# Performance work log

Measured on AMD Instinct MI355X. Metric: run time of the kernel, lower is better.

The kernel has to match this reference:

```python
import jax, jax.numpy as jnp
import numpy as np

IN_F = 512
OUT_F = 512
ALPHA = 0.2  # LeakyReLU negative slope
# dropout p=0.1 is a no-op at inference (training=False), so omitted


def setup_inputs() -> dict:
    key = jax.random.key(0)
    k1, k2, k3 = jax.random.split(key, 3)
    B, N = 16, 1024
    x = jax.random.normal(k1, (B, N, IN_F), dtype=jnp.float32)
    # xavier_uniform with gain=1.414
    limW = 1.414 * np.sqrt(6.0 / (IN_F + OUT_F))
    W = jax.random.uniform(k2, (IN_F, OUT_F), minval=-limW, maxval=limW, dtype=jnp.float32)
    lima = 1.414 * np.sqrt(6.0 / (2 * OUT_F + 1))
    a = jax.random.uniform(k3, (2 * OUT_F, 1), minval=-lima, maxval=lima, dtype=jnp.float32)
    beta = jnp.ones((1,), dtype=jnp.float32)
    return {"x": x, "W": W, "a": a, "beta": beta}


def reference(x, W, a, beta):
    # h: [B, N, F]
    h = jnp.matmul(x, W)
    # Split attention vector: e_ij = leakyrelu(h_i . a1 + h_j . a2)
    a1 = a[:OUT_F, 0]   # [F]
    a2 = a[OUT_F:, 0]   # [F]
    s1 = jnp.einsum('bnf,f->bn', h, a1)  # [B, N]
    s2 = jnp.einsum('bnf,f->bn', h, a2)  # [B, N]
    e = s1[:, :, None] + s2[:, None, :]  # [B, N, N]
    e = jnp.where(e > 0, e, ALPHA * e)   # LeakyReLU
    attention = jax.nn.softmax(e, axis=2)
    h_prime = jnp.einsum('bnm,bmf->bnf', attention, h)
    out = jax.nn.elu(h_prime + beta * h)
    return out
```

## Files before the change

### kernel.cpp

```cpp
#include <hip/hip_runtime.h>

using u16 = unsigned short;
using u32 = unsigned int;

#define ALPHA 0.2f
#define LOG2E 1.4426950408889634f

typedef __bf16 bf16x8 __attribute__((ext_vector_type(8)));
typedef float f32x4 __attribute__((ext_vector_type(4)));
typedef float f32x16 __attribute__((ext_vector_type(16)));

__device__ __forceinline__ u16 f2bf(float f) {
  u32 u = __builtin_bit_cast(u32, f);
  u += 0x7FFFu + ((u >> 16) & 1u);
  return (u16)(u >> 16);
}
__device__ __forceinline__ float bf2f(u16 h) {
  u32 u = ((u32)h) << 16;
  return __builtin_bit_cast(float, u);
}
__device__ __forceinline__ void gload_lds16(const void* g, void* l) {
  __builtin_amdgcn_global_load_lds((__attribute__((address_space(1))) void*)g,
                                   (__attribute__((address_space(3))) void*)l,
                                   16, 0, 0);
}

__global__ __launch_bounds__(256) void k_cast_wT(const float* __restrict__ W, u16* __restrict__ wbt) {
  int idx = blockIdx.x * 256 + threadIdx.x;
  int k = idx >> 9, n = idx & 511;
  wbt[n * 512 + k] = f2bf(W[idx]);
}


__global__ __launch_bounds__(256, 2) void k_gemm1(const float* __restrict__ x, const u16* __restrict__ wbt,
                                                  const float* __restrict__ a,
                                                  u16* __restrict__ hbf, u16* __restrict__ hbt2,
                                                  float* __restrict__ s1p, float* __restrict__ s2p) {
  __shared__ __attribute__((aligned(16))) char lds[73728];
  __shared__ __attribute__((aligned(16))) float a_l[256];

  const int t = threadIdx.x;
  const int lane = t & 63;
  const int w = t >> 6;
  const int l31 = lane & 31, lhi = lane >> 5;
  const int rb = w >> 1, cg = w & 1;
  const int g = blockIdx.x;
  const int cb = (g >> 3) & 3;
  const int tile_m = (g & 7) | ((g >> 5) << 3);
  const int row0 = tile_m * 128;
  const int col0 = cb * 128;

  a_l[t] = (t < 128) ? a[col0 + t] : a[512 + col0 + (t - 128)];

  f32x16 acc[2][2];
#pragma unroll
  for (int i = 0; i < 2; ++i)
#pragma unroll
    for (int j = 0; j < 2; ++j)
#pragma unroll
      for (int r = 0; r < 16; ++r) acc[i][j][r] = 0.f;

#define STAGE_G1(kt, Ab, Bb)                                                              \
  {                                                                                       \
    const int k0_ = (kt) * 32;                                                            \
    _Pragma("unroll")                                                                     \
    for (int i = 0; i < 4; ++i) {                                                         \
      int G = i * 256 + t;                                                                \
      int row = G >> 3, ks = G & 7;                                                       \
      gload_lds16(x + (size_t)(row0 + row) * 512 + k0_ + ((ks ^ (row & 7)) * 4),          \
                  (Ab) + (size_t)(i * 256 + w * 64) * 16);                                \
    }                                                                                     \
    _Pragma("unroll")                                                                     \
    for (int i = 0; i < 2; ++i) {                                                         \
      int G = i * 256 + t;                                                                \
      int col = G >> 2, ks = G & 3;                                                       \
      gload_lds16(wbt + (size_t)(col0 + col) * 512 + k0_ + ((ks ^ ((col >> 1) & 3)) * 8), \
                  (Bb) + (size_t)(i * 256 + w * 64) * 16);                                \
    }                                                                                     \
  }

#define COMPUTE_G1(Ab, Bb)                                                                         \
  {                                                                                                \
    _Pragma("unroll")                                                                              \
    for (int ks = 0; ks < 2; ++ks) {                                                               \
      bf16x8 af[2];                                                                                \
      _Pragma("unroll")                                                                            \
      for (int sub = 0; sub < 2; ++sub) {                                                          \
        const int arow = rb * 64 + sub * 32 + l31;                                                 \
        const int kg = ks * 4 + lhi * 2;                                                           \
        f32x4 fa0 = *reinterpret_cast<const f32x4*>((Ab) + (size_t)(arow * 8 + (kg ^ (arow & 7))) * 16); \
        f32x4 fa1 = *reinterpret_cast<const f32x4*>((Ab) + (size_t)(arow * 8 + ((kg + 1) ^ (arow & 7))) * 16); \
        _Pragma("unroll")                                                                          \
        for (int jj = 0; jj < 4; ++jj) {                                                           \
          af[sub][jj] = (__bf16)fa0[jj];                                                           \
          af[sub][jj + 4] = (__bf16)fa1[jj];                                                       \
        }                                                                                          \
      }                                                                                            \
      bf16x8 bfr[2];                                                                               \
      _Pragma("unroll")                                                                            \
      for (int bt = 0; bt < 2; ++bt) {                                                             \
        const int bcol = cg * 64 + bt * 32 + l31;                                                  \
        const int kslot = (ks * 2 + lhi) ^ ((bcol >> 1) & 3);                                      \
        bfr[bt] = *reinterpret_cast<const bf16x8*>((Bb) + (size_t)(bcol * 4 + kslot) * 16);        \
      }                                                                                            \
      _Pragma("unroll")                                                                            \
      for (int sub = 0; sub < 2; ++sub)                                                            \
        _Pragma("unroll")                                                                          \
        for (int bt = 0; bt < 2; ++bt)                                                             \
          acc[sub][bt] = __builtin_amdgcn_mfma_f32_32x32x16_bf16(af[sub], bfr[bt], acc[sub][bt], 0, 0, 0); \
    }                                                                                              \
  }

  char* Ac = lds;             char* Bc = lds + 49152;
  char* An = lds + 16384;     char* Bn = lds + 57344;
  char* As = lds + 32768;     char* Bs = lds + 65536;

  STAGE_G1(0, Ac, Bc);
  STAGE_G1(1, An, Bn);
  __builtin_amdgcn_sched_barrier(0);
  asm volatile("s_waitcnt vmcnt(6) lgkmcnt(0)" ::: "memory");
  __builtin_amdgcn_s_barrier();
  __builtin_amdgcn_sched_barrier(0);

#pragma unroll 1
  for (int kt = 0; kt < 14; ++kt) {
    STAGE_G1(kt + 2, As, Bs);
    COMPUTE_G1(Ac, Bc);
    __builtin_amdgcn_sched_barrier(0);
    asm volatile("s_waitcnt vmcnt(6)" ::: "memory");
    __builtin_amdgcn_s_barrier();
    __builtin_amdgcn_sched_barrier(0);
    char* ta = Ac; Ac = An; An = As; As = ta;
    char* tb = Bc; Bc = Bn; Bn = Bs; Bs = tb;
  }
  COMPUTE_G1(Ac, Bc);
  __builtin_amdgcn_sched_barrier(0);
  asm volatile("s_waitcnt vmcnt(0)" ::: "memory");
  __builtin_amdgcn_s_barrier();
  __builtin_amdgcn_sched_barrier(0);
  COMPUTE_G1(An, Bn);
#undef STAGE_G1
#undef COMPUTE_G1

  __syncthreads();

  u16* lT = (u16*)lds;
#pragma unroll
  for (int sub = 0; sub < 2; ++sub)
#pragma unroll
    for (int bt = 0; bt < 2; ++bt) {
      const int col = cg * 64 + bt * 32 + l31;
#pragma unroll
      for (int r = 0; r < 16; ++r) {
        int row = rb * 64 + sub * 32 + (r & 3) + 8 * (r >> 2) + 4 * lhi;
        lT[row * 136 + col] = f2bf(acc[sub][bt][r]);
      }
    }
  __syncthreads();

#pragma unroll
  for (int i = 0; i < 8; ++i) {
    int G = i * 256 + t;
    int row = G >> 4, gg = G & 15;
    uint4 v = *reinterpret_cast<const uint4*>(&lT[row * 136 + gg * 8]);
    *reinterpret_cast<uint4*>(&hbf[(size_t)(row0 + row) * 512 + col0 + gg * 8]) = v;
  }
  const int bb = row0 >> 10;
  const int nb = row0 & 1023;
  u16* hb2 = hbt2 + (size_t)bb * 524288;
#pragma unroll
  for (int i = 0; i < 8; ++i) {
    int G = i * 256 + t;
    int col = G & 127, rg = G >> 7;
    u32 wd[4];
#pragma unroll
    for (int jj = 0; jj < 4; ++jj) {
      u16 lo = lT[(rg * 8 + 2 * jj) * 136 + col];
      u16 hi = lT[(rg * 8 + 2 * jj + 1) * 136 + col];
      wd[jj] = (u32)lo | ((u32)hi << 16);
    }
    uint4 o = {wd[0], wd[1], wd[2], wd[3]};
    const int m0 = nb + rg * 8;
    const int f = col0 + col;
    size_t idx = (size_t)(m0 >> 4) * 8192 + (size_t)(f >> 5) * 512 + (size_t)((m0 >> 3) & 1) * 256 + (size_t)(f & 31) * 8;
    *reinterpret_cast<uint4*>(&hb2[idx]) = o;
  }
  {
    const int r2 = t >> 1, half = t & 1;
    float d1 = 0.f, d2 = 0.f;
#pragma unroll
    for (int i = 0; i < 8; ++i) {
      uint4 v = *reinterpret_cast<const uint4*>(&lT[r2 * 136 + half * 64 + i * 8]);
      u32 wds[4] = {v.x, v.y, v.z, v.w};
#pragma unroll
      for (int jj = 0; jj < 8; ++jj) {
        float h = bf2f((u16)(wds[jj >> 1] >> ((jj & 1) * 16)));
        d1 += h * a_l[half * 64 + i * 8 + jj];
        d2 += h * a_l[128 + half * 64 + i * 8 + jj];
      }
    }
    d1 += __shfl_xor(d1, 1);
    d2 += __shfl_xor(d2, 1);
    if (half == 0) {
      s1p[cb * 16384 + row0 + r2] = d1;
      s2p[cb * 16384 + row0 + r2] = d2;
    }
  }
}

__global__ __launch_bounds__(256) void k_reduce(const float* __restrict__ s1p, const float* __restrict__ s2p,
                                                float* __restrict__ s1L, float* __restrict__ s2L) {
  int id = blockIdx.x * 256 + threadIdx.x;
  float d1 = s1p[id] + s1p[16384 + id] + s1p[32768 + id] + s1p[49152 + id];
  float d2 = s2p[id] + s2p[16384 + id] + s2p[32768 + id] + s2p[49152 + id];
  s1L[id] = d1 * LOG2E;
  s2L[id] = d2 * LOG2E;
}

__global__ __launch_bounds__(256, 3) void k_attn(const u16* __restrict__ hbt2, const u16* __restrict__ hbf,
                                                 const float* __restrict__ s1Lg, const float* __restrict__ s2Lg,
                                                 const float* __restrict__ betag, float* __restrict__ out) {
  __shared__ __attribute__((aligned(16))) float e1_l[1024];
  __shared__ __attribute__((aligned(16))) float e2_l[1024];
  const int t = threadIdx.x;
  const int lane = t & 63;
  const int w = t >> 6;
  const int fl = lane & 15;
  const int mg = lane >> 4;

  const int B = blockIdx.x;
  const int b = (B & 7) * 2 + ((B >> 3) & 1);
  const int j = B >> 4;
  const int n0 = (j >> 2) * 64;
  const int c0 = (j & 3) * 128;

  const u16* hb2 = hbt2 + (size_t)b * 524288;

  for (int i = t; i < 1024; i += 256) {
    float v = s2Lg[b * 1024 + i];
    e1_l[i] = exp2f(v);
    e2_l[i] = exp2f(ALPHA * v);
  }

  const int myrow = n0 + w * 16 + fl;
  const float s1v = s1Lg[b * 1024 + myrow];
  const float c1 = exp2f(s1v), c2 = exp2f(ALPHA * s1v);

  f32x4 acc[8];
#pragma unroll
  for (int ct = 0; ct < 8; ++ct) acc[ct] = (f32x4){0.f, 0.f, 0.f, 0.f};
  f32x4 accs = (f32x4){0.f, 0.f, 0.f, 0.f};
  bf16x8 ones;
#pragma unroll
  for (int q = 0; q < 8; ++q) ones[q] = (__bf16)1.0f;

  __syncthreads();

  const u16* bp = hb2 + (size_t)(c0 >> 5) * 512 + (size_t)(mg >> 1) * 8192 + (size_t)(mg & 1) * 256 + (size_t)fl * 8;
  const int mgo = mg * 8;

#define LOAD_B(dst, s)                                                                          \
  {                                                                                             \
    const u16* np_ = bp + (size_t)(s) * 16384;                                                  \
    _Pragma("unroll")                                                                           \
    for (int ct = 0; ct < 8; ++ct)                                                              \
      dst[ct] = *reinterpret_cast<const bf16x8*>(np_ + (ct >> 1) * 512 + (ct & 1) * 128);       \
  }

#define STEP_ATTN(s, buf)                                                       \
  {                                                                             \
    const int mo = (s) * 32 + mgo;                                              \
    f32x4 ea = *reinterpret_cast<const f32x4*>(&e1_l[mo]);                      \
    f32x4 eb = *reinterpret_cast<const f32x4*>(&e1_l[mo + 4]);                  \
    f32x4 fa = *reinterpret_cast<const f32x4*>(&e2_l[mo]);                      \
    f32x4 fb = *reinterpret_cast<const f32x4*>(&e2_l[mo + 4]);                  \
    bf16x8 af;                                                                  \
    _Pragma("unroll")                                                           \
    for (int q = 0; q < 4; ++q) {                                               \
      af[q] = (__bf16)fmaxf(c1 * ea[q], c2 * fa[q]);                            \
      af[q + 4] = (__bf16)fmaxf(c1 * eb[q], c2 * fb[q]);                        \
    }                                                                           \
    accs = __builtin_amdgcn_mfma_f32_16x16x32_bf16(af, ones, accs, 0, 0, 0);    \
    _Pragma("unroll")                                                           \
    for (int ct = 0; ct < 8; ++ct)                                              \
      acc[ct] = __builtin_amdgcn_mfma_f32_16x16x32_bf16(af, (buf)[ct], acc[ct], 0, 0, 0); \
  }

  bf16x8 P0[8], P1[8], P2[8];
  LOAD_B(P0, 0);
  LOAD_B(P1, 1);
  LOAD_B(P2, 2);

#pragma unroll 1
  for (int s = 0; s < 30; s += 3) {
    STEP_ATTN(s + 0, P0); LOAD_B(P0, (s + 3) & 31);
    STEP_ATTN(s + 1, P1); LOAD_B(P1, (s + 4) & 31);
    STEP_ATTN(s + 2, P2); LOAD_B(P2, (s + 5) & 31);
  }
  STEP_ATTN(30, P0);
  STEP_ATTN(31, P1);
#undef LOAD_B
#undef STEP_ATTN

  const float beta = betag[0];
  const u16* hf = hbf + (size_t)b * 1024 * 512;
  f32x4 iv;
#pragma unroll
  for (int q = 0; q < 4; ++q) iv[q] = 1.0f / accs[q];
  const int rowb = n0 + w * 16 + (lane >> 4) * 4;
#pragma unroll
  for (int ct = 0; ct < 8; ++ct) {
    const int colv = c0 + ct * 16 + fl;
#pragma unroll
    for (int q = 0; q < 4; ++q) {
      float hv = bf2f(hf[(size_t)(rowb + q) * 512 + colv]);
      float xv = acc[ct][q] * iv[q] + beta * hv;
      out[((size_t)b * 1024 + rowb + q) * 512 + colv] = xv > 0.f ? xv : __expf(xv) - 1.0f;
    }
  }
}

extern "C" void kernel_launch(void* const* d_in, const int* in_sizes, int n_in,
                              void* d_out, int out_size, void* d_ws, size_t ws_size,
                              hipStream_t stream) {
  const float* x = (const float*)d_in[0];
  const float* W = (const float*)d_in[1];
  const float* a = (const float*)d_in[2];
  const float* beta = (const float*)d_in[3];
  float* out = (float*)d_out;

  char* ws = (char*)d_ws;
  u16* hbf = (u16*)ws;
  u16* hbt2 = (u16*)(ws + (16u << 20));
  u16* wbt = (u16*)(ws + (32u << 20));
  float* s1p = (float*)(ws + (32u << 20) + (512u << 10));
  float* s2p = (float*)(ws + (32u << 20) + (768u << 10));
  float* s1L = (float*)(ws + (33u << 20));
  float* s2L = (float*)(ws + (33u << 20) + (64u << 10));

  k_cast_wT<<<1024, 256, 0, stream>>>(W, wbt);
  k_gemm1<<<512, 256, 0, stream>>>(x, wbt, a, hbf, hbt2, s1p, s2p);
  k_reduce<<<64, 256, 0, stream>>>(s1p, s2p, s1L, s2L);
  k_attn<<<1024, 256, 0, stream>>>(hbt2, hbf, s1L, s2L, beta, out);
}
```

Before: 67.81 us.

## Switch attention kernel to 32x32x16 MFMA with larger row tiles per wave

```diff
diff --git a/kernel.cpp b/kernel.cpp
--- a/kernel.cpp
+++ b/kernel.cpp
@@ -217,107 +217,130 @@
   s2L[id] = d2 * LOG2E;
 }
 
-__global__ __launch_bounds__(256, 3) void k_attn(const u16* __restrict__ hbt2, const u16* __restrict__ hbf,
+__global__ __launch_bounds__(128, 1) void k_attn(const u16* __restrict__ hbt2, const u16* __restrict__ hbf,
                                                  const float* __restrict__ s1Lg, const float* __restrict__ s2Lg,
                                                  const float* __restrict__ betag, float* __restrict__ out) {
   __shared__ __attribute__((aligned(16))) float e1_l[1024];
   __shared__ __attribute__((aligned(16))) float e2_l[1024];
+  __shared__ __attribute__((aligned(16))) float inv_l[128];
   const int t = threadIdx.x;
   const int lane = t & 63;
   const int w = t >> 6;
-  const int fl = lane & 15;
-  const int mg = lane >> 4;
+  const int l31 = lane & 31, lhi = lane >> 5;
 
   const int B = blockIdx.x;
   const int b = (B & 7) * 2 + ((B >> 3) & 1);
   const int j = B >> 4;
-  const int n0 = (j >> 2) * 64;
+  const int n0 = (j >> 2) * 128;
   const int c0 = (j & 3) * 128;
 
   const u16* hb2 = hbt2 + (size_t)b * 524288;
 
-  for (int i = t; i < 1024; i += 256) {
+  for (int i = t; i < 1024; i += 128) {
     float v = s2Lg[b * 1024 + i];
     e1_l[i] = exp2f(v);
     e2_l[i] = exp2f(ALPHA * v);
   }
 
-  const int myrow = n0 + w * 16 + fl;
-  const float s1v = s1Lg[b * 1024 + myrow];
-  const float c1 = exp2f(s1v), c2 = exp2f(ALPHA * s1v);
-
-  f32x4 acc[8];
-#pragma unroll
-  for (int ct = 0; ct < 8; ++ct) acc[ct] = (f32x4){0.f, 0.f, 0.f, 0.f};
-  f32x4 accs = (f32x4){0.f, 0.f, 0.f, 0.f};
-  bf16x8 ones;
-#pragma unroll
-  for (int q = 0; q < 8; ++q) ones[q] = (__bf16)1.0f;
+  const float s1a = s1Lg[b * 1024 + n0 + w * 64 + l31];
+  const float s1b = s1Lg[b * 1024 + n0 + w * 64 + 32 + l31];
+  const float c1a = exp2f(s1a), c2a = exp2f(ALPHA * s1a);
+  const float c1b = exp2f(s1b), c2b = exp2f(ALPHA * s1b);
+
+  f32x16 acc0[4], acc1[4];
+#pragma unroll
+  for (int ct = 0; ct < 4; ++ct) {
+#pragma unroll
+    for (int r = 0; r < 16; ++r) { acc0[ct][r] = 0.f; acc1[ct][r] = 0.f; }
+  }
+  float psum0 = 0.f, psum1 = 0.f;
 
   __syncthreads();
 
-  const u16* bp = hb2 + (size_t)(c0 >> 5) * 512 + (size_t)(mg >> 1) * 8192 + (size_t)(mg & 1) * 256 + (size_t)fl * 8;
-  const int mgo = mg * 8;
-
-#define LOAD_B(dst, s)                                                                          \
-  {                                                                                             \
-    const u16* np_ = bp + (size_t)(s) * 16384;                                                  \
-    _Pragma("unroll")                                                                           \
-    for (int ct = 0; ct < 8; ++ct)                                                              \
-      dst[ct] = *reinterpret_cast<const bf16x8*>(np_ + (ct >> 1) * 512 + (ct & 1) * 128);       \
+  const u16* bp = hb2 + (size_t)(c0 >> 5) * 512 + (size_t)(lhi * 32 + l31) * 8;
+
+#define LOAD_B(dst, s)                                                                         \
+  {                                                                                            \
+    const u16* np_ = bp + (size_t)(s) * 8192;                                                  \
+    _Pragma("unroll")                                                                          \
+    for (int ct = 0; ct < 4; ++ct) dst[ct] = *reinterpret_cast<const bf16x8*>(np_ + ct * 512); \
   }
 
 #define STEP_ATTN(s, buf)                                                       \
   {                                                                             \
-    const int mo = (s) * 32 + mgo;                                              \
+    const int mo = (s) * 16 + lhi * 8;                                          \
     f32x4 ea = *reinterpret_cast<const f32x4*>(&e1_l[mo]);                      \
     f32x4 eb = *reinterpret_cast<const f32x4*>(&e1_l[mo + 4]);                  \
     f32x4 fa = *reinterpret_cast<const f32x4*>(&e2_l[mo]);                      \
     f32x4 fb = *reinterpret_cast<const f32x4*>(&e2_l[mo + 4]);                  \
-    bf16x8 af;                                                                  \
+    bf16x8 af0, af1;                                                            \
     _Pragma("unroll")                                                           \
     for (int q = 0; q < 4; ++q) {                                               \
-      af[q] = (__bf16)fmaxf(c1 * ea[q], c2 * fa[q]);                            \
-      af[q + 4] = (__bf16)fmaxf(c1 * eb[q], c2 * fb[q]);                        \
+      float pa0 = fmaxf(c1a * ea[q], c2a * fa[q]);                              \
+      float pa1 = fmaxf(c1a * eb[q], c2a * fb[q]);                              \
+      float pb0 = fmaxf(c1b * ea[q], c2b * fa[q]);                              \
+      float pb1 = fmaxf(c1b * eb[q], c2b * fb[q]);                              \
+      psum0 += pa0 + pa1;                                                       \
+      psum1 += pb0 + pb1;                                                       \
+      af0[q] = (__bf16)pa0; af0[q + 4] = (__bf16)pa1;                           \
+      af1[q] = (__bf16)pb0; af1[q + 4] = (__bf16)pb1;                           \
     }                                                                           \
-    accs = __builtin_amdgcn_mfma_f32_16x16x32_bf16(af, ones, accs, 0, 0, 0);    \
     _Pragma("unroll")                                                           \
-    for (int ct = 0; ct < 8; ++ct)                                              \
-      acc[ct] = __builtin_amdgcn_mfma_f32_16x16x32_bf16(af, (buf)[ct], acc[ct], 0, 0, 0); \
-  }
-
-  bf16x8 P0[8], P1[8], P2[8];
+    for (int ct = 0; ct < 4; ++ct) {                                            \
+      acc0[ct] = __builtin_amdgcn_mfma_f32_32x32x16_bf16(af0, (buf)[ct], acc0[ct], 0, 0, 0); \
+      acc1[ct] = __builtin_amdgcn_mfma_f32_32x32x16_bf16(af1, (buf)[ct], acc1[ct], 0, 0, 0); \
+    }                                                                           \
+  }
+
+  bf16x8 P0[4], P1[4], P2[4];
   LOAD_B(P0, 0);
   LOAD_B(P1, 1);
   LOAD_B(P2, 2);
 
 #pragma unroll 1
-  for (int s = 0; s < 30; s += 3) {
-    STEP_ATTN(s + 0, P0); LOAD_B(P0, (s + 3) & 31);
-    STEP_ATTN(s + 1, P1); LOAD_B(P1, (s + 4) & 31);
-    STEP_ATTN(s + 2, P2); LOAD_B(P2, (s + 5) & 31);
-  }
-  STEP_ATTN(30, P0);
-  STEP_ATTN(31, P1);
+  for (int s = 0; s < 63; s += 3) {
+    STEP_ATTN(s + 0, P0); LOAD_B(P0, (s + 3) & 63);
+    STEP_ATTN(s + 1, P1); LOAD_B(P1, (s + 4) & 63);
+    STEP_ATTN(s + 2, P2); LOAD_B(P2, (s + 5) & 63);
+  }
+  STEP_ATTN(63, P0);
 #undef LOAD_B
 #undef STEP_ATTN
 
+  psum0 += __shfl_xor(psum0, 32);
+  psum1 += __shfl_xor(psum1, 32);
+  if (lhi == 0) {
+    inv_l[w * 64 + l31] = 1.0f / psum0;
+    inv_l[w * 64 + 32 + l31] = 1.0f / psum1;
+  }
+  __syncthreads();
+
   const float beta = betag[0];
   const u16* hf = hbf + (size_t)b * 1024 * 512;
-  f32x4 iv;
-#pragma unroll
-  for (int q = 0; q < 4; ++q) iv[q] = 1.0f / accs[q];
-  const int rowb = n0 + w * 16 + (lane >> 4) * 4;
-#pragma unroll
-  for (int ct = 0; ct < 8; ++ct) {
-    const int colv = c0 + ct * 16 + fl;
-#pragma unroll
-    for (int q = 0; q < 4; ++q) {
-      float hv = bf2f(hf[(size_t)(rowb + q) * 512 + colv]);
-      float xv = acc[ct][q] * iv[q] + beta * hv;
-      out[((size_t)b * 1024 + rowb + q) * 512 + colv] = xv > 0.f ? xv : __expf(xv) - 1.0f;
-    }
-  }
+
+#define EPILOGUE(ACC, RG)                                                                 \
+  {                                                                                       \
+    _Pragma("unroll")                                                                     \
+    for (int rg4 = 0; rg4 < 4; ++rg4) {                                                   \
+      const int rl = rg4 * 8 + lhi * 4;                                                   \
+      const int rowb = n0 + w * 64 + (RG) * 32 + rl;                                      \
+      f32x4 iv = *reinterpret_cast<const f32x4*>(&inv_l[w * 64 + (RG) * 32 + rl]);        \
+      _Pragma("unroll")                                                                   \
+      for (int ct = 0; ct < 4; ++ct) {                                                    \
+        const int colv = c0 + ct * 32 + l31;                                              \
+        _Pragma("unroll")                                                                 \
+        for (int q = 0; q < 4; ++q) {                                                     \
+          float hv = bf2f(hf[(size_t)(rowb + q) * 512 + colv]);                           \
+          float xv = ACC[ct][rg4 * 4 + q] * iv[q] + beta * hv;                            \
+          out[((size_t)b * 1024 + rowb + q) * 512 + colv] = xv > 0.f ? xv : __expf(xv) - 1.0f; \
+        }                                                                                 \
+      }                                                                                   \
+    }                                                                                     \
+  }
+
+  EPILOGUE(acc0, 0);
+  EPILOGUE(acc1, 1);
+#undef EPILOGUE
 }
 
 extern "C" void kernel_launch(void* const* d_in, const int* in_sizes, int n_in,
@@ -341,5 +364,5 @@
   k_cast_wT<<<1024, 256, 0, stream>>>(W, wbt);
   k_gemm1<<<512, 256, 0, stream>>>(x, wbt, a, hbf, hbt2, s1p, s2p);
   k_reduce<<<64, 256, 0, stream>>>(s1p, s2p, s1L, s2L);
-  k_attn<<<1024, 256, 0, stream>>>(hbt2, hbf, s1L, s2L, beta, out);
-}
+  k_attn<<<512, 128, 0, stream>>>(hbt2, hbf, s1L, s2L, beta, out);
+}
```

New measurement: 62.46 us. 7.9% less time.
